# Kernel tuning notes

Hardware: AMD Instinct MI355X
Metric: run time of the kernel (lower is better)

## Reference

```python
import jax, jax.numpy as jnp
import numpy as np

D_MODEL = 1024
N_HEADS = 16
HEAD_DIM = D_MODEL // N_HEADS


def setup_inputs() -> dict:
    key = jax.random.key(0)
    k1, k2, k3 = jax.random.split(key, 3)
    B, T, C = 4, 2048, D_MODEL
    x = jax.random.normal(k1, (B, T, C), dtype=jnp.float32)
    # torch Linear weight is (out,in); store as (in,out) so y = x @ W
    w_qkv = jax.random.normal(k2, (C, 3 * C), dtype=jnp.float32) * (1.0 / np.sqrt(C))
    w_proj = jax.random.normal(k3, (C, C), dtype=jnp.float32) * (1.0 / np.sqrt(C))
    return {"x": x, "w_qkv": w_qkv, "w_proj": w_proj}


def reference(x, w_qkv, w_proj):
    B, T, C = x.shape
    H, Dh = N_HEADS, HEAD_DIM
    qkv = x @ w_qkv                        # (B,T,3C)
    q, k, v = jnp.split(qkv, 3, axis=-1)
    def heads(t):
        return t.reshape(B, T, H, Dh).transpose(0, 2, 1, 3)  # (B,H,T,Dh)
    q, k, v = heads(q), heads(k), heads(v)
    scores = jnp.einsum('bhqd,bhkd->bhqk', q, k) / np.sqrt(Dh).astype(np.float32)
    causal = jnp.tril(jnp.ones((T, T), dtype=bool))
    scores = jnp.where(causal, scores, -jnp.inf)
    attn = jax.nn.softmax(scores, axis=-1)
    y = jnp.einsum('bhqk,bhkd->bhqd', attn, v)  # (B,H,T,Dh)
    y = y.transpose(0, 2, 1, 3).reshape(B, T, C)
    return y @ w_proj
```

## Files before the change

### kernel.cpp

```cpp
#include <hip/hip_runtime.h>

#define SEQ_T 2048
#define NBATCH 4
#define CDIM 1024
#define NHEAD 16
#define MROWS 8192
#define QKVC 3072

typedef unsigned short u16;
typedef __bf16 bf16x8 __attribute__((ext_vector_type(8)));
typedef float f32x4 __attribute__((ext_vector_type(4)));
typedef unsigned short u16x8 __attribute__((ext_vector_type(8)));
typedef unsigned uint32x4 __attribute__((ext_vector_type(4)));

__device__ __forceinline__ u16 f32_to_bf16(float f) {
  union { float f; unsigned int u; } v; v.f = f;
  unsigned int u = v.u;
  unsigned int r = ((u >> 16) & 1u) + 0x7fffu;
  return (u16)((u + r) >> 16);
}

__device__ __forceinline__ void gload_lds16(const u16* g, u16* l) {
  __builtin_amdgcn_global_load_lds(
      (const __attribute__((address_space(1))) void*)g,
      (__attribute__((address_space(3))) void*)l, 16, 0, 0);
}


__global__ __launch_bounds__(256) void cast_block_kernel(const float* __restrict__ in,
                                                         u16* __restrict__ out) {
  const int i = blockIdx.x * 256 + threadIdx.x;
  const int kg = i & 127;
  const int row = i >> 7;
  const float4 v0 = ((const float4*)in)[i * 2];
  const float4 v1 = ((const float4*)in)[i * 2 + 1];
  union { u16 u[8]; bf16x8 b; } o;
  o.u[0] = f32_to_bf16(v0.x); o.u[1] = f32_to_bf16(v0.y);
  o.u[2] = f32_to_bf16(v0.z); o.u[3] = f32_to_bf16(v0.w);
  o.u[4] = f32_to_bf16(v1.x); o.u[5] = f32_to_bf16(v1.y);
  o.u[6] = f32_to_bf16(v1.z); o.u[7] = f32_to_bf16(v1.w);
  const int tile = (row >> 4) * 32 + (kg >> 2);
  const int lane = (row & 15) + ((kg & 3) << 4);
  *(bf16x8*)(out + (size_t)tile * 512 + lane * 8) = o.b;
}

__global__ void transpose_cast_block_kernel(const float* __restrict__ in,
                                            u16* __restrict__ out) {
  __shared__ float tile[32][33];
  const int c0 = blockIdx.x * 32, r0 = blockIdx.y * 32;
  const int tx = threadIdx.x, ty = threadIdx.y;
  #pragma unroll
  for (int i = 0; i < 32; i += 8)
    tile[ty + i][tx] = in[(size_t)(r0 + ty + i) * QKVC + c0 + tx];
  __syncthreads();
  const int t = ty * 32 + tx;
  if (t < 128) {
    const int cc = t & 31, kgq = t >> 5;
    union { u16 u[8]; bf16x8 b; } o;
    #pragma unroll
    for (int j = 0; j < 8; ++j) o.u[j] = f32_to_bf16(tile[kgq * 8 + j][cc]);
    const int rowN = c0 + cc;
    const int tileI = (rowN >> 4) * 32 + (r0 >> 5);
    const int lane = (rowN & 15) + (kgq << 4);
    *(bf16x8*)(out + (size_t)tileI * 512 + lane * 8) = o.b;
  }
}

__global__ void transpose_cast_kernel(const float* __restrict__ in, u16* __restrict__ out,
                                      int R, int Cc) {
  __shared__ float tile[32][33];
  int c0 = blockIdx.x * 32, r0 = blockIdx.y * 32;
  int tx = threadIdx.x, ty = threadIdx.y;
  #pragma unroll
  for (int i = 0; i < 32; i += 8)
    tile[ty + i][tx] = in[(size_t)(r0 + ty + i) * Cc + c0 + tx];
  __syncthreads();
  #pragma unroll
  for (int i = 0; i < 32; i += 8)
    out[(size_t)(c0 + ty + i) * R + r0 + tx] = f32_to_bf16(tile[tx][ty + i]);
}

__global__ __launch_bounds__(256) void repack_k_kernel(const u16* __restrict__ QKV,
                                                       u16* __restrict__ Kc) {
  const int kvt32 = blockIdx.x, bh = blockIdx.y;
  const int b = bh >> 4, h = bh & 15;
  const int tid = threadIdx.x;
  const int f = tid >> 6, l = tid & 63;
  const int t = f >> 1, i = f & 1;
  const int row = kvt32 * 32 + t * 16 + (l & 15);
  const bf16x8 v = *(const bf16x8*)(QKV + (size_t)b * SEQ_T * QKVC + (size_t)row * QKVC +
                                    CDIM + h * 64 + i * 32 + (l >> 4) * 8);
  *(bf16x8*)(Kc + (size_t)bh * 131072 + (size_t)kvt32 * 2048 + f * 512 + l * 8) = v;
}

__global__ void repack_v_kernel(const u16* __restrict__ QKV, u16* __restrict__ Vc) {
  __shared__ u16 tile[32][34];
  const int t0 = blockIdx.x * 32, d0 = blockIdx.y * 32;
  const int bh = blockIdx.z;
  const int b = bh >> 4, h = bh & 15;
  const int tx = threadIdx.x, ty = threadIdx.y;
  const u16* Vp = QKV + (size_t)b * SEQ_T * QKVC + 2 * CDIM + h * 64 + d0;
  #pragma unroll
  for (int i = 0; i < 32; i += 8)
    tile[ty + i][tx] = Vp[(size_t)(t0 + ty + i) * QKVC + tx];
  __syncthreads();
  const int tid = ty * 32 + tx;
  if (tid < 128) {
    const int bc = tid >> 2, ag = tid & 3;
    union { u16 u[8]; bf16x8 v; } o;
    #pragma unroll
    for (int j = 0; j < 8; ++j) o.u[j] = tile[ag * 8 + j][bc];
    const int dvl = d0 + bc;
    *(bf16x8*)(Vc + (size_t)bh * 131072 + (size_t)(t0 >> 5) * 2048 +
               (dvl >> 4) * 512 + ag * 128 + (dvl & 15) * 8) = o.v;
  }
}

template <bool QSCALE>
__global__ __launch_bounds__(512, 2)
void gemm256_kernel(const u16* __restrict__ Ab, const u16* __restrict__ Bb,
                    u16* __restrict__ C, int N) {
  __shared__ u16 sA[3][8192];
  __shared__ u16 sB[3][8192];
  const int tid = threadIdx.x;
  const int lane = tid & 63, w = tid >> 6;
  const int wm = w >> 2, wn = w & 3;
  const int l15 = lane & 15, lhi = lane >> 4;
  const int row0 = blockIdx.x * 256, col0 = blockIdx.y * 256;

  const u16* aT0 = Ab + ((size_t)((row0 >> 4) + w)     * 32) * 512 + lane * 8;
  const u16* aT1 = Ab + ((size_t)((row0 >> 4) + 8 + w) * 32) * 512 + lane * 8;
  const u16* bT0 = Bb + ((size_t)((col0 >> 4) + w)     * 32) * 512 + lane * 8;
  const u16* bT1 = Bb + ((size_t)((col0 >> 4) + 8 + w) * 32) * 512 + lane * 8;

  f32x4 acc[8][4] = {};

#define STAGE(KT, S)                                                            \
  {                                                                             \
    gload_lds16(aT0 + (size_t)(KT) * 512, &sA[S][w * 512]);                     \
    gload_lds16(aT1 + (size_t)(KT) * 512, &sA[S][(8 + w) * 512]);               \
    gload_lds16(bT0 + (size_t)(KT) * 512, &sB[S][w * 512]);                     \
    gload_lds16(bT1 + (size_t)(KT) * 512, &sB[S][(8 + w) * 512]);               \
  }
#define COMPUTE(S)                                                              \
  {                                                                             \
    bf16x8 bf[4];                                                               \
    _Pragma("unroll") for (int ni = 0; ni < 4; ++ni)                            \
      bf[ni] = *(const bf16x8*)&sB[S][(wn * 4 + ni) * 512 + lane * 8];          \
    __builtin_amdgcn_s_setprio(1);                                              \
    _Pragma("unroll") for (int mi = 0; mi < 8; ++mi) {                          \
      const bf16x8 af = *(const bf16x8*)&sA[S][(wm * 8 + mi) * 512 + lane * 8]; \
      _Pragma("unroll") for (int ni = 0; ni < 4; ++ni)                          \
        acc[mi][ni] = __builtin_amdgcn_mfma_f32_16x16x32_bf16(af, bf[ni],       \
                                                              acc[mi][ni], 0, 0, 0); \
    }                                                                           \
    __builtin_amdgcn_s_setprio(0);                                              \
  }
#define WAITBAR4                                                                \
  asm volatile("s_waitcnt vmcnt(4)" ::: "memory");                              \
  __builtin_amdgcn_sched_barrier(0);                                            \
  __builtin_amdgcn_s_barrier();

  STAGE(0, 0);
  STAGE(1, 1);
  WAITBAR4;

  #pragma unroll 1
  for (int kt = 0; kt < 30; kt += 3) {
    STAGE(kt + 2, 2); COMPUTE(0); WAITBAR4;
    STAGE(kt + 3, 0); COMPUTE(1); WAITBAR4;
    STAGE(kt + 4, 1); COMPUTE(2); WAITBAR4;
  }
  COMPUTE(0);
  asm volatile("s_waitcnt vmcnt(0)" ::: "memory");
  __builtin_amdgcn_sched_barrier(0);
  __builtin_amdgcn_s_barrier();
  COMPUTE(1);
#undef STAGE
#undef COMPUTE
#undef WAITBAR4

  #pragma unroll
  for (int mi = 0; mi < 8; ++mi)
    #pragma unroll
    for (int ni = 0; ni < 4; ++ni)
      #pragma unroll
      for (int r = 0; r < 4; ++r) {
        const int rr = row0 + wm * 128 + mi * 16 + lhi * 4 + r;
        const int cc = col0 + wn * 64 + ni * 16 + l15;
        float v = acc[mi][ni][r];
        if (QSCALE && cc < CDIM) v *= 0.18033688011f;
        C[(size_t)rr * N + cc] = f32_to_bf16(v);
      }
}

template <typename OT, bool QSCALE>
__global__ __launch_bounds__(256, 3)
void gemm_bt_kernel(const u16* __restrict__ A, const u16* __restrict__ Bt,
                    OT* __restrict__ C, int N, int K) {
  __shared__ u16 sA[3][4096];
  __shared__ u16 sB[3][4096];
  const int tid = threadIdx.x;
  const int lane = tid & 63, w = tid >> 6;
  const int wm = w >> 1, wn = w & 1;
  const int l15 = lane & 15, lhi = lane >> 4;
  const int row0 = blockIdx.x * 128, col0 = blockIdx.y * 128;

  const int oln  = ((lane & 3) - (lane >> 2)) & 3;
  const int srow = w * 32 + (lane >> 2);
  const u16* aS = A  + (size_t)(row0 + srow) * K + oln * 8;
  const u16* bS = Bt + (size_t)(col0 + srow) * K + oln * 8;
  const int stD = w * 1024;
  const int rdA = (wm * 64 + l15) * 32 + ((lhi + l15) & 3) * 8;
  const int rdB = (wn * 64 + l15) * 32 + ((lhi + l15) & 3) * 8;

  f32x4 acc[4][4] = {};

#define STAGE(KT, S)                                                            \
  {                                                                             \
    const size_t ko = (size_t)(KT) * 32;                                        \
    gload_lds16(aS + ko,          &sA[S][stD]);                                 \
    gload_lds16(aS + ko + 16 * K, &sA[S][stD + 512]);                           \
    gload_lds16(bS + ko,          &sB[S][stD]);                                 \
    gload_lds16(bS + ko + 16 * K, &sB[S][stD + 512]);                           \
  }
#define COMPUTE(S)                                                              \
  {                                                                             \
    bf16x8 af[4], bf[4];                                                        \
    _Pragma("unroll") for (int mi = 0; mi < 4; ++mi)                            \
      af[mi] = *(const bf16x8*)&sA[S][rdA + mi * 512];                          \
    _Pragma("unroll") for (int ni = 0; ni < 4; ++ni)                            \
      bf[ni] = *(const bf16x8*)&sB[S][rdB + ni * 512];                          \
    __builtin_amdgcn_s_setprio(1);                                              \
    _Pragma("unroll") for (int mi = 0; mi < 4; ++mi)                            \
      _Pragma("unroll") for (int ni = 0; ni < 4; ++ni)                          \
        acc[mi][ni] = __builtin_amdgcn_mfma_f32_16x16x32_bf16(af[mi], bf[ni],   \
                                                              acc[mi][ni], 0, 0, 0); \
    __builtin_amdgcn_s_setprio(0);                                              \
  }
#define WAITBAR4                                                                \
  asm volatile("s_waitcnt vmcnt(4)" ::: "memory");                              \
  __builtin_amdgcn_sched_barrier(0);                                            \
  __builtin_amdgcn_s_barrier();

  STAGE(0, 0);
  STAGE(1, 1);
  WAITBAR4;

  #pragma unroll 1
  for (int kt = 0; kt < 30; kt += 3) {
    STAGE(kt + 2, 2); COMPUTE(0); WAITBAR4;
    STAGE(kt + 3, 0); COMPUTE(1); WAITBAR4;
    STAGE(kt + 4, 1); COMPUTE(2); WAITBAR4;
  }
  COMPUTE(0);
  asm volatile("s_waitcnt vmcnt(0)" ::: "memory");
  __builtin_amdgcn_sched_barrier(0);
  __builtin_amdgcn_s_barrier();
  COMPUTE(1);
#undef STAGE
#undef COMPUTE
#undef WAITBAR4

  #pragma unroll
  for (int mt = 0; mt < 4; ++mt)
    #pragma unroll
    for (int nt = 0; nt < 4; ++nt)
      #pragma unroll
      for (int r = 0; r < 4; ++r) {
        const int rr = row0 + wm * 64 + mt * 16 + lhi * 4 + r;
        const int cc = col0 + wn * 64 + nt * 16 + l15;
        float v = acc[mt][nt][r];
        if (QSCALE && cc < CDIM) v *= 0.18033688011f;
        if constexpr (sizeof(OT) == 2) C[(size_t)rr * N + cc] = f32_to_bf16(v);
        else                           C[(size_t)rr * N + cc] = v;
      }
}

template <bool DOMASK>
__device__ __forceinline__ void attn_step(const bf16x8 (&qf)[2],
                                          const bf16x8 (&kf)[2][2],
                                          const bf16x8 (&vb)[4],
                                          const bf16x8 ones,
                                          f32x4 (&acc)[4], f32x4& acc1,
                                          int l15, int lhi, int kv0, int qg) {
  f32x4 st[2];
  #pragma unroll
  for (int t = 0; t < 2; ++t) {
    f32x4 z = {0.f, 0.f, 0.f, 0.f};
    z = __builtin_amdgcn_mfma_f32_16x16x32_bf16(kf[t][0], qf[0], z, 0, 0, 0);
    z = __builtin_amdgcn_mfma_f32_16x16x32_bf16(kf[t][1], qf[1], z, 0, 0, 0);
    st[t] = z;
  }
  #pragma unroll
  for (int t = 0; t < 2; ++t)
    #pragma unroll
    for (int r = 0; r < 4; ++r) {
      float sv = st[t][r];
      if (DOMASK) {
        const int kvg = kv0 + t * 16 + lhi * 4 + r;
        sv = (kvg > qg) ? -__builtin_inff() : sv;
      }
      st[t][r] = exp2f(sv);
    }
  unsigned c00, c01, c10, c11;
  asm("v_cvt_pk_bf16_f32 %0, %1, %2" : "=v"(c00) : "v"(st[0][0]), "v"(st[0][1]));
  asm("v_cvt_pk_bf16_f32 %0, %1, %2" : "=v"(c01) : "v"(st[0][2]), "v"(st[0][3]));
  asm("v_cvt_pk_bf16_f32 %0, %1, %2" : "=v"(c10) : "v"(st[1][0]), "v"(st[1][1]));
  asm("v_cvt_pk_bf16_f32 %0, %1, %2" : "=v"(c11) : "v"(st[1][2]), "v"(st[1][3]));
  asm("v_permlane32_swap_b32 %0, %1" : "+v"(c00), "+v"(c10));
  asm("v_permlane32_swap_b32 %0, %1" : "+v"(c01), "+v"(c11));
  asm("v_permlane16_swap_b32 %0, %1" : "+v"(c00), "+v"(c10));
  asm("v_permlane16_swap_b32 %0, %1" : "+v"(c01), "+v"(c11));
  uint32x4 pw; pw[0] = c00; pw[1] = c01; pw[2] = c10; pw[3] = c11;
  const bf16x8 pa = __builtin_bit_cast(bf16x8, pw);
  #pragma unroll
  for (int d = 0; d < 4; ++d)
    acc[d] = __builtin_amdgcn_mfma_f32_16x16x32_bf16(pa, vb[d], acc[d], 0, 0, 0);
  acc1 = __builtin_amdgcn_mfma_f32_16x16x32_bf16(pa, ones, acc1, 0, 0, 0);
}

__global__ __launch_bounds__(256, 4) void attn_kernel(const u16* __restrict__ QKV,
                                                      const u16* __restrict__ Kc,
                                                      const u16* __restrict__ Vc,
                                                      u16* __restrict__ Y) {
  __shared__ u16 Kl[2][2048];
  __shared__ u16 Vl[2][2048];
  const int tid = threadIdx.x, lane = tid & 63, wid = tid >> 6;
  const int l15 = lane & 15, lhi = lane >> 4;
  const int id = blockIdx.x;
  const int xcd = id & 7, k = (id >> 3) & 15, hi3 = id >> 7;
  const int bh = hi3 * 8 + xcd;
  const int b = bh >> 4, h = bh & 15;
  const int pa = k * 4 + wid;
  const int qA0 = pa * 16, qB0 = (127 - pa) * 16;
  const int nchA = pa / 2 + 1, nchB = (127 - pa) / 2 + 1;
  const int ncmax = (127 - k * 4) / 2 + 1;
  const size_t base = (size_t)b * SEQ_T * QKVC;
  const u16* Qp  = QKV + base + h * 64;
  const u16* KcC = Kc + (size_t)bh * 131072;
  const u16* VcC = Vc + (size_t)bh * 131072;

  u16x8 ou;
  #pragma unroll
  for (int j = 0; j < 8; ++j) ou[j] = 0x3F80;
  const bf16x8 ones = __builtin_bit_cast(bf16x8, ou);

  gload_lds16(KcC + wid * 512 + lane * 8, &Kl[0][wid * 512]);
  gload_lds16(VcC + wid * 512 + lane * 8, &Vl[0][wid * 512]);

  bf16x8 qfA[2], qfB[2];
  #pragma unroll
  for (int i = 0; i < 2; ++i) {
    qfA[i] = *(const bf16x8*)(Qp + (size_t)(qA0 + l15) * QKVC + i * 32 + lhi * 8);
    qfB[i] = *(const bf16x8*)(Qp + (size_t)(qB0 + l15) * QKVC + i * 32 + lhi * 8);
  }
  const int qgA = qA0 + l15, qgB = qB0 + l15;

  f32x4 accA[4] = {}, accB[4] = {};
  f32x4 acc1A = {}, acc1B = {};

  __syncthreads();

  int cbuf = 0;
  for (int ic = 0; ic < ncmax; ++ic) {
    if (ic + 1 < ncmax) {
      const u16* kg = KcC + (size_t)(ic + 1) * 2048 + wid * 512 + lane * 8;
      const u16* vg = VcC + (size_t)(ic + 1) * 2048 + wid * 512 + lane * 8;
      gload_lds16(kg, &Kl[cbuf ^ 1][wid * 512]);
      gload_lds16(vg, &Vl[cbuf ^ 1][wid * 512]);
    }
    const u16* kb = &Kl[cbuf][0];
    const u16* vp = &Vl[cbuf][0];
    bf16x8 kf[2][2], vb[4];
    #pragma unroll
    for (int t = 0; t < 2; ++t)
      #pragma unroll
      for (int i = 0; i < 2; ++i)
        kf[t][i] = *(const bf16x8*)(kb + (t * 2 + i) * 512 + lane * 8);
    #pragma unroll
    for (int d = 0; d < 4; ++d)
      vb[d] = *(const bf16x8*)(vp + d * 512 + lane * 8);

    const int kv0 = ic * 32;
    if (ic < nchB) {
      if (ic == nchB - 1)
        attn_step<true>(qfB, kf, vb, ones, accB, acc1B, l15, lhi, kv0, qgB);
      else
        attn_step<false>(qfB, kf, vb, ones, accB, acc1B, l15, lhi, kv0, qgB);
    }
    if (ic < nchA) {
      if (ic == nchA - 1)
        attn_step<true>(qfA, kf, vb, ones, accA, acc1A, l15, lhi, kv0, qgA);
      else
        attn_step<false>(qfA, kf, vb, ones, accA, acc1A, l15, lhi, kv0, qgA);
    }
    __syncthreads();
    cbuf ^= 1;
  }

  u16* Yp = Y + (size_t)b * SEQ_T * CDIM + h * 64;
  #pragma unroll
  for (int r = 0; r < 4; ++r) {
    const float ivA = 1.0f / acc1A[r];
    const float ivB = 1.0f / acc1B[r];
    #pragma unroll
    for (int d = 0; d < 4; ++d) {
      Yp[(size_t)(qA0 + lhi * 4 + r) * CDIM + d * 16 + l15] = f32_to_bf16(accA[d][r] * ivA);
      Yp[(size_t)(qB0 + lhi * 4 + r) * CDIM + d * 16 + l15] = f32_to_bf16(accB[d][r] * ivB);
    }
  }
}

extern "C" void kernel_launch(void* const* d_in, const int* in_sizes, int n_in,
                              void* d_out, int out_size, void* d_ws, size_t ws_size,
                              hipStream_t stream) {
  const float* x      = (const float*)d_in[0];
  const float* w_qkv  = (const float*)d_in[1];
  const float* w_proj = (const float*)d_in[2];
  float* out = (float*)d_out;

  u16* Xb  = (u16*)d_ws;
  u16* Wqt = Xb  + (size_t)MROWS * CDIM;
  u16* Wpt = Wqt + (size_t)QKVC * CDIM;
  u16* QKV = Wpt + (size_t)CDIM * CDIM;
  u16* Yb  = QKV + (size_t)MROWS * QKVC;
  u16* Vc  = Yb  + (size_t)MROWS * CDIM;
  u16* Kc  = Xb;

  cast_block_kernel<<<MROWS * CDIM / 8 / 256, 256, 0, stream>>>(x, Xb);
  transpose_cast_block_kernel<<<dim3(QKVC / 32, CDIM / 32), dim3(32, 8), 0, stream>>>(w_qkv, Wqt);
  transpose_cast_kernel<<<dim3(CDIM / 32, CDIM / 32), dim3(32, 8), 0, stream>>>(w_proj, Wpt, CDIM, CDIM);

  gemm256_kernel<true><<<dim3(MROWS / 256, QKVC / 256), 512, 0, stream>>>(Xb, Wqt, QKV, QKVC);

  repack_k_kernel<<<dim3(SEQ_T / 32, NBATCH * NHEAD), 256, 0, stream>>>(QKV, Kc);
  repack_v_kernel<<<dim3(SEQ_T / 32, 2, NBATCH * NHEAD), dim3(32, 8), 0, stream>>>(QKV, Vc);

  attn_kernel<<<1024, 256, 0, stream>>>(QKV, Kc, Vc, Yb);

  gemm_bt_kernel<float, false><<<dim3(MROWS / 128, CDIM / 128), 256, 0, stream>>>(Yb, Wpt, out, CDIM, CDIM);
}
```

Measured before the change: 194.3 us.

## Fuse K/V repacking into QKV GEMM epilogue with 128x128 tiles

The QKV projection GEMM now writes Q directly, pre-scaled, into a compact Q buffer. K and V tiles are staged through LDS in the epilogue and written straight into the attention-ready Kc and Vc layouts. This removes the two separate repack kernels and the full QKV intermediate round-trip through memory. The GEMM also drops from 256x256 tiles with 512 threads to 128x128 tiles with 256 threads, which may lower per-block reuse but gives more blocks.

```diff
diff --git a/kernel.cpp b/kernel.cpp
--- a/kernel.cpp
+++ b/kernel.cpp
@@ -80,80 +80,43 @@
     out[(size_t)(c0 + ty + i) * R + r0 + tx] = f32_to_bf16(tile[tx][ty + i]);
 }
 
-__global__ __launch_bounds__(256) void repack_k_kernel(const u16* __restrict__ QKV,
-                                                       u16* __restrict__ Kc) {
-  const int kvt32 = blockIdx.x, bh = blockIdx.y;
-  const int b = bh >> 4, h = bh & 15;
-  const int tid = threadIdx.x;
-  const int f = tid >> 6, l = tid & 63;
-  const int t = f >> 1, i = f & 1;
-  const int row = kvt32 * 32 + t * 16 + (l & 15);
-  const bf16x8 v = *(const bf16x8*)(QKV + (size_t)b * SEQ_T * QKVC + (size_t)row * QKVC +
-                                    CDIM + h * 64 + i * 32 + (l >> 4) * 8);
-  *(bf16x8*)(Kc + (size_t)bh * 131072 + (size_t)kvt32 * 2048 + f * 512 + l * 8) = v;
-}
-
-__global__ void repack_v_kernel(const u16* __restrict__ QKV, u16* __restrict__ Vc) {
-  __shared__ u16 tile[32][34];
-  const int t0 = blockIdx.x * 32, d0 = blockIdx.y * 32;
-  const int bh = blockIdx.z;
-  const int b = bh >> 4, h = bh & 15;
-  const int tx = threadIdx.x, ty = threadIdx.y;
-  const u16* Vp = QKV + (size_t)b * SEQ_T * QKVC + 2 * CDIM + h * 64 + d0;
-  #pragma unroll
-  for (int i = 0; i < 32; i += 8)
-    tile[ty + i][tx] = Vp[(size_t)(t0 + ty + i) * QKVC + tx];
-  __syncthreads();
-  const int tid = ty * 32 + tx;
-  if (tid < 128) {
-    const int bc = tid >> 2, ag = tid & 3;
-    union { u16 u[8]; bf16x8 v; } o;
-    #pragma unroll
-    for (int j = 0; j < 8; ++j) o.u[j] = tile[ag * 8 + j][bc];
-    const int dvl = d0 + bc;
-    *(bf16x8*)(Vc + (size_t)bh * 131072 + (size_t)(t0 >> 5) * 2048 +
-               (dvl >> 4) * 512 + ag * 128 + (dvl & 15) * 8) = o.v;
-  }
-}
-
-template <bool QSCALE>
-__global__ __launch_bounds__(512, 2)
-void gemm256_kernel(const u16* __restrict__ Ab, const u16* __restrict__ Bb,
-                    u16* __restrict__ C, int N) {
-  __shared__ u16 sA[3][8192];
-  __shared__ u16 sB[3][8192];
+__global__ __launch_bounds__(256, 3)
+void gemm1_kernel(const u16* __restrict__ Ab, const u16* __restrict__ Bb,
+                  u16* __restrict__ Qb, u16* __restrict__ Kc, u16* __restrict__ Vc) {
+  __shared__ u16 lds[24576];
   const int tid = threadIdx.x;
   const int lane = tid & 63, w = tid >> 6;
-  const int wm = w >> 2, wn = w & 3;
+  const int wm = w >> 1, wn = w & 1;
   const int l15 = lane & 15, lhi = lane >> 4;
-  const int row0 = blockIdx.x * 256, col0 = blockIdx.y * 256;
-
-  const u16* aT0 = Ab + ((size_t)((row0 >> 4) + w)     * 32) * 512 + lane * 8;
-  const u16* aT1 = Ab + ((size_t)((row0 >> 4) + 8 + w) * 32) * 512 + lane * 8;
-  const u16* bT0 = Bb + ((size_t)((col0 >> 4) + w)     * 32) * 512 + lane * 8;
-  const u16* bT1 = Bb + ((size_t)((col0 >> 4) + 8 + w) * 32) * 512 + lane * 8;
-
-  f32x4 acc[8][4] = {};
-
+  const int row0 = blockIdx.x * 128, col0 = blockIdx.y * 128;
+  const int rt0 = row0 >> 4, ct0 = col0 >> 4;
+
+  const u16* aT = Ab + (size_t)(rt0 + w * 2) * 16384 + lane * 8;
+  const u16* bT = Bb + (size_t)(ct0 + w * 2) * 16384 + lane * 8;
+
+  f32x4 acc[4][4] = {};
+
+#define SA(S) (lds + (S) * 4096)
+#define SB(S) (lds + 12288 + (S) * 4096)
 #define STAGE(KT, S)                                                            \
   {                                                                             \
-    gload_lds16(aT0 + (size_t)(KT) * 512, &sA[S][w * 512]);                     \
-    gload_lds16(aT1 + (size_t)(KT) * 512, &sA[S][(8 + w) * 512]);               \
-    gload_lds16(bT0 + (size_t)(KT) * 512, &sB[S][w * 512]);                     \
-    gload_lds16(bT1 + (size_t)(KT) * 512, &sB[S][(8 + w) * 512]);               \
+    gload_lds16(aT + (size_t)(KT) * 512,         SA(S) + (w * 2) * 512);        \
+    gload_lds16(aT + 16384 + (size_t)(KT) * 512, SA(S) + (w * 2 + 1) * 512);    \
+    gload_lds16(bT + (size_t)(KT) * 512,         SB(S) + (w * 2) * 512);        \
+    gload_lds16(bT + 16384 + (size_t)(KT) * 512, SB(S) + (w * 2 + 1) * 512);    \
   }
 #define COMPUTE(S)                                                              \
   {                                                                             \
-    bf16x8 bf[4];                                                               \
+    bf16x8 af[4], bf[4];                                                        \
+    _Pragma("unroll") for (int mi = 0; mi < 4; ++mi)                            \
+      af[mi] = *(const bf16x8*)(SA(S) + (wm * 4 + mi) * 512 + lane * 8);        \
     _Pragma("unroll") for (int ni = 0; ni < 4; ++ni)                            \
-      bf[ni] = *(const bf16x8*)&sB[S][(wn * 4 + ni) * 512 + lane * 8];          \
+      bf[ni] = *(const bf16x8*)(SB(S) + (wn * 4 + ni) * 512 + lane * 8);        \
     __builtin_amdgcn_s_setprio(1);                                              \
-    _Pragma("unroll") for (int mi = 0; mi < 8; ++mi) {                          \
-      const bf16x8 af = *(const bf16x8*)&sA[S][(wm * 8 + mi) * 512 + lane * 8]; \
+    _Pragma("unroll") for (int mi = 0; mi < 4; ++mi)                            \
       _Pragma("unroll") for (int ni = 0; ni < 4; ++ni)                          \
-        acc[mi][ni] = __builtin_amdgcn_mfma_f32_16x16x32_bf16(af, bf[ni],       \
+        acc[mi][ni] = __builtin_amdgcn_mfma_f32_16x16x32_bf16(af[mi], bf[ni],   \
                                                               acc[mi][ni], 0, 0, 0); \
-    }                                                                           \
     __builtin_amdgcn_s_setprio(0);                                              \
   }
 #define WAITBAR4                                                                \
@@ -179,25 +142,71 @@
 #undef STAGE
 #undef COMPUTE
 #undef WAITBAR4
-
-  #pragma unroll
-  for (int mi = 0; mi < 8; ++mi)
-    #pragma unroll
-    for (int ni = 0; ni < 4; ++ni)
-      #pragma unroll
-      for (int r = 0; r < 4; ++r) {
-        const int rr = row0 + wm * 128 + mi * 16 + lhi * 4 + r;
-        const int cc = col0 + wn * 64 + ni * 16 + l15;
-        float v = acc[mi][ni][r];
-        if (QSCALE && cc < CDIM) v *= 0.18033688011f;
-        C[(size_t)rr * N + cc] = f32_to_bf16(v);
+#undef SA
+#undef SB
+
+  const int region = col0 >> 10;
+  if (region == 0) {
+    #pragma unroll
+    for (int mt = 0; mt < 4; ++mt)
+      #pragma unroll
+      for (int nt = 0; nt < 4; ++nt)
+        #pragma unroll
+        for (int r = 0; r < 4; ++r) {
+          const int rr = row0 + wm * 64 + mt * 16 + lhi * 4 + r;
+          const int cc = col0 + wn * 64 + nt * 16 + l15;
+          Qb[(size_t)rr * CDIM + cc] = f32_to_bf16(acc[mt][nt][r] * 0.18033688011f);
+        }
+  } else {
+    __syncthreads();
+    if (region == 1) {
+      #pragma unroll
+      for (int mt = 0; mt < 4; ++mt)
+        #pragma unroll
+        for (int nt = 0; nt < 4; ++nt)
+          #pragma unroll
+          for (int r = 0; r < 4; ++r) {
+            const int sidx = (wn * 4 + wm * 2 + (mt >> 1)) * 2048
+                           + ((mt & 1) * 2 + (nt >> 1)) * 512
+                           + ((nt & 1) * 2 + (l15 >> 3)) * 128
+                           + (lhi * 4 + r) * 8 + (l15 & 7);
+            lds[sidx] = f32_to_bf16(acc[mt][nt][r]);
+          }
+    } else {
+      #pragma unroll
+      for (int mt = 0; mt < 4; ++mt)
+        #pragma unroll
+        for (int nt = 0; nt < 4; ++nt)
+          #pragma unroll
+          for (int r = 0; r < 4; ++r) {
+            const int sidx = (wn * 4 + wm * 2 + (mt >> 1)) * 2048
+                           + nt * 512
+                           + ((mt & 1) * 2 + (lhi >> 1)) * 128
+                           + l15 * 8 + (lhi & 1) * 4 + r;
+            lds[sidx] = f32_to_bf16(acc[mt][nt][r]);
+          }
+    }
+    __syncthreads();
+    u16* dstB = (region == 1) ? Kc : Vc;
+    const int bb = row0 >> 11;
+    const int kv0b = (row0 & 2047) >> 5;
+    const int hbase = (col0 & 1023) >> 6;
+    #pragma unroll
+    for (int hh = 0; hh < 2; ++hh) {
+      u16* dst = dstB + (size_t)(bb * 16 + hbase + hh) * 131072 + (size_t)kv0b * 2048;
+      const u16* src = lds + hh * 8192;
+      #pragma unroll
+      for (int c = 0; c < 4; ++c) {
+        const int o = (c * 256 + tid) * 8;
+        *(uint32x4*)(dst + o) = *(const uint32x4*)(src + o);
       }
-}
-
-template <typename OT, bool QSCALE>
+    }
+  }
+}
+
 __global__ __launch_bounds__(256, 3)
-void gemm_bt_kernel(const u16* __restrict__ A, const u16* __restrict__ Bt,
-                    OT* __restrict__ C, int N, int K) {
+void gemm2_kernel(const u16* __restrict__ A, const u16* __restrict__ Bt,
+                  float* __restrict__ C, int N, int K) {
   __shared__ u16 sA[3][4096];
   __shared__ u16 sB[3][4096];
   const int tid = threadIdx.x;
@@ -270,10 +279,7 @@
       for (int r = 0; r < 4; ++r) {
         const int rr = row0 + wm * 64 + mt * 16 + lhi * 4 + r;
         const int cc = col0 + wn * 64 + nt * 16 + l15;
-        float v = acc[mt][nt][r];
-        if (QSCALE && cc < CDIM) v *= 0.18033688011f;
-        if constexpr (sizeof(OT) == 2) C[(size_t)rr * N + cc] = f32_to_bf16(v);
-        else                           C[(size_t)rr * N + cc] = v;
+        C[(size_t)rr * N + cc] = acc[mt][nt][r];
       }
 }
 
@@ -320,7 +326,7 @@
   acc1 = __builtin_amdgcn_mfma_f32_16x16x32_bf16(pa, ones, acc1, 0, 0, 0);
 }
 
-__global__ __launch_bounds__(256, 4) void attn_kernel(const u16* __restrict__ QKV,
+__global__ __launch_bounds__(256, 4) void attn_kernel(const u16* __restrict__ Qb,
                                                       const u16* __restrict__ Kc,
                                                       const u16* __restrict__ Vc,
                                                       u16* __restrict__ Y) {
@@ -336,8 +342,7 @@
   const int qA0 = pa * 16, qB0 = (127 - pa) * 16;
   const int nchA = pa / 2 + 1, nchB = (127 - pa) / 2 + 1;
   const int ncmax = (127 - k * 4) / 2 + 1;
-  const size_t base = (size_t)b * SEQ_T * QKVC;
-  const u16* Qp  = QKV + base + h * 64;
+  const u16* Qp  = Qb + (size_t)b * SEQ_T * CDIM + h * 64;
   const u16* KcC = Kc + (size_t)bh * 131072;
   const u16* VcC = Vc + (size_t)bh * 131072;
 
@@ -352,8 +357,8 @@
   bf16x8 qfA[2], qfB[2];
   #pragma unroll
   for (int i = 0; i < 2; ++i) {
-    qfA[i] = *(const bf16x8*)(Qp + (size_t)(qA0 + l15) * QKVC + i * 32 + lhi * 8);
-    qfB[i] = *(const bf16x8*)(Qp + (size_t)(qB0 + l15) * QKVC + i * 32 + lhi * 8);
+    qfA[i] = *(const bf16x8*)(Qp + (size_t)(qA0 + l15) * CDIM + i * 32 + lhi * 8);
+    qfB[i] = *(const bf16x8*)(Qp + (size_t)(qB0 + l15) * CDIM + i * 32 + lhi * 8);
   }
   const int qgA = qA0 + l15, qgB = qB0 + l15;
 
@@ -423,21 +428,18 @@
   u16* Xb  = (u16*)d_ws;
   u16* Wqt = Xb  + (size_t)MROWS * CDIM;
   u16* Wpt = Wqt + (size_t)QKVC * CDIM;
-  u16* QKV = Wpt + (size_t)CDIM * CDIM;
-  u16* Yb  = QKV + (size_t)MROWS * QKVC;
-  u16* Vc  = Yb  + (size_t)MROWS * CDIM;
-  u16* Kc  = Xb;
+  u16* Qb  = Wpt + (size_t)CDIM * CDIM;
+  u16* Kc  = Qb  + (size_t)MROWS * CDIM;
+  u16* Vc  = Kc  + (size_t)64 * 131072;
+  u16* Yb  = Vc  + (size_t)64 * 131072;
 
   cast_block_kernel<<<MROWS * CDIM / 8 / 256, 256, 0, stream>>>(x, Xb);
   transpose_cast_block_kernel<<<dim3(QKVC / 32, CDIM / 32), dim3(32, 8), 0, stream>>>(w_qkv, Wqt);
   transpose_cast_kernel<<<dim3(CDIM / 32, CDIM / 32), dim3(32, 8), 0, stream>>>(w_proj, Wpt, CDIM, CDIM);
 
-  gemm256_kernel<true><<<dim3(MROWS / 256, QKVC / 256), 512, 0, stream>>>(Xb, Wqt, QKV, QKVC);
-
-  repack_k_kernel<<<dim3(SEQ_T / 32, NBATCH * NHEAD), 256, 0, stream>>>(QKV, Kc);
-  repack_v_kernel<<<dim3(SEQ_T / 32, 2, NBATCH * NHEAD), dim3(32, 8), 0, stream>>>(QKV, Vc);
-
-  attn_kernel<<<1024, 256, 0, stream>>>(QKV, Kc, Vc, Yb);
-
-  gemm_bt_kernel<float, false><<<dim3(MROWS / 128, CDIM / 128), 256, 0, stream>>>(Yb, Wpt, out, CDIM, CDIM);
-}
+  gemm1_kernel<<<dim3(MROWS / 128, QKVC / 128), 256, 0, stream>>>(Xb, Wqt, Qb, Kc, Vc);
+
+  attn_kernel<<<1024, 256, 0, stream>>>(Qb, Kc, Vc, Yb);
+
+  gemm2_kernel<<<dim3(MROWS / 128, CDIM / 128), 256, 0, stream>>>(Yb, Wpt, out, CDIM, CDIM);
+}
```

New measurement: 167.4 us. 1.16x faster.
